# Kernel optimization log

Measured on AMD Instinct MI355X. Metric: run time of the kernel, lower is better.

Reference implementation:

```python
import jax, jax.numpy as jnp
import numpy as np

B, S, H = 8, 1024, 1024
NH, HD = 16, 64
MBANK, TOPK = 128, 16
NLAYERS, FF = 12, 4096
EPS = 1e-5


def _ln(x, w, b):
    m = x.mean(-1, keepdims=True)
    v = ((x - m) ** 2).mean(-1, keepdims=True)
    return (x - m) / jnp.sqrt(v + EPS) * w + b


def _split_heads(x):  # [B,S,H] -> [B,NH,S,HD]
    return x.reshape(B, S, NH, HD).transpose(0, 2, 1, 3)


def _sdpa(q, k, v):  # inputs [B,NH,S,HD]
    scores = jnp.einsum('bhqd,bhkd->bhqk', q, k) / jnp.sqrt(jnp.float32(HD))
    attn = jax.nn.softmax(scores, axis=-1)
    o = jnp.einsum('bhqk,bhkd->bhqd', attn, v)
    return o.transpose(0, 2, 1, 3).reshape(B, S, H)


def setup_inputs() -> dict:
    key = jax.random.key(0)
    ks = jax.random.split(key, 24)
    n = lambda k, shp, s=0.02: jax.random.normal(k, shp, jnp.float32) * s
    return {
        'hidden_states': jax.random.normal(ks[0], (B, S, H), jnp.float32),
        'ln1_w': jnp.ones((H,), jnp.float32), 'ln1_b': jnp.zeros((H,), jnp.float32),
        'ln2_w': jnp.ones((H,), jnp.float32), 'ln2_b': jnp.zeros((H,), jnp.float32),
        'rec_wq': n(ks[1], (H, H)), 'rec_wk': n(ks[2], (H, H)),
        'rec_wv': n(ks[3], (H, H)), 'rec_wo': n(ks[4], (H, H)),
        'rec_ad_w1': n(ks[5], (H // 4, H)), 'rec_ad_w2': n(ks[6], (H, H // 4)),
        'mem_bank': n(ks[7], (MBANK, H)),
        'alloc_w': n(ks[8], (MBANK, H)), 'alloc_b': jnp.zeros((MBANK,), jnp.float32),
        'retr_w': n(ks[9], (MBANK, H)), 'retr_b': jnp.zeros((MBANK,), jnp.float32),
        'upd_w': n(ks[10], (H, H)), 'upd_b': jnp.zeros((H,), jnp.float32),
        'mem_scales': jnp.full((NLAYERS,), 0.1, jnp.float32),
        'attn_in_w': n(ks[11], (3 * H, H)), 'attn_in_b': jnp.zeros((3 * H,), jnp.float32),
        'attn_out_w': n(ks[12], (H, H)), 'attn_out_b': jnp.zeros((H,), jnp.float32),
        'mlp_w1': n(ks[13], (FF, H)), 'mlp_b1': jnp.zeros((FF,), jnp.float32),
        'mlp_w2': n(ks[14], (H, FF)), 'mlp_b2': jnp.zeros((H,), jnp.float32),
        'layer_idx': 4,
    }


def reference(hidden_states, ln1_w, ln1_b, ln2_w, ln2_b,
              rec_wq, rec_wk, rec_wv, rec_wo, rec_ad_w1, rec_ad_w2,
              mem_bank, alloc_w, alloc_b, retr_w, retr_b, upd_w, upd_b, mem_scales,
              attn_in_w, attn_in_b, attn_out_w, attn_out_b,
              mlp_w1, mlp_b1, mlp_w2, mlp_b2, layer_idx):
    residual = hidden_states
    h = _ln(hidden_states, ln1_w, ln1_b)

    # --- CrossLayerParameterRecycler (layer_idx % 4 == 0 and > 0 -> recycle) ---
    if layer_idx % 4 == 0 and layer_idx > 0:
        q = _split_heads(h @ rec_wq.T)
        k = _split_heads(h @ rec_wk.T)
        v = _split_heads(h @ rec_wv.T)
        base_out = _sdpa(q, k, v) @ rec_wo.T
        h = jax.nn.relu(base_out @ rec_ad_w1.T) @ rec_ad_w2.T

    # --- CrossLayerMemoryManager ---
    pooled = h.mean(axis=1)                                  # [B,H]
    alloc_weights = jax.nn.softmax(pooled @ alloc_w.T + alloc_b, axis=-1)   # [B,MBANK]
    retr_weights = jax.nn.softmax(pooled @ retr_w.T + retr_b, axis=-1)
    retrieved = retr_weights @ mem_bank                      # [B,H]
    h = h + retrieved[:, None, :] * mem_scales[layer_idx]
    update_signals = jax.nn.sigmoid(h.mean(axis=1) @ upd_w.T + upd_b)       # [B,H]
    _, top_idx = jax.lax.top_k(alloc_weights, TOPK)          # [B,TOPK]

    # sequential per-batch scatter (later batches overwrite earlier, as in torch loop)
    def _write(mb, be):
        idx, sig = be
        return mb.at[idx].set(jnp.broadcast_to(sig, (TOPK, H))), None
    new_mem_bank, _ = jax.lax.scan(_write, mem_bank, (top_idx, update_signals))

    # --- self attention (nn.MultiheadAttention, batch_first) ---
    qkv = h @ attn_in_w.T + attn_in_b                        # [B,S,3H]
    q, k, v = jnp.split(qkv, 3, axis=-1)
    attn_out = _sdpa(_split_heads(q), _split_heads(k), _split_heads(v))
    attn_out = attn_out @ attn_out_w.T + attn_out_b
    h = residual + attn_out

    # --- MLP block ---
    residual2 = h
    h = _ln(h, ln2_w, ln2_b)
    h = jax.nn.gelu(h @ mlp_w1.T + mlp_b1, approximate=False) @ mlp_w2.T + mlp_b2
    out = residual2 + h
    return out, new_mem_bank
```

## Files before the change

### kernel.cpp

```cpp
#include <hip/hip_runtime.h>
#include <hip/hip_bf16.h>
#include <math.h>
#include <stdint.h>


#define BB 8
#define SS 1024
#define HH 1024
#define NHEAD 16
#define HD 64
#define MBANK 128
#define TOPK_N 16
#define FF_DIM 4096
#define MROWS (BB * SS)
#define NB_ELEM (8ull*1024*1024)

typedef __bf16 bf16x8 __attribute__((ext_vector_type(8)));
typedef __bf16 bf16x4 __attribute__((ext_vector_type(4)));
typedef float f32x4 __attribute__((ext_vector_type(4)));

#define SCALE_LOG2E 0.18033688011112042f

__device__ __forceinline__ unsigned short f2b(float x) {
  unsigned u = __float_as_uint(x);
  unsigned r = (u + 0x7FFFu + ((u >> 16) & 1u)) >> 16;
  return (unsigned short)r;
}
__device__ __forceinline__ float b2f(unsigned short u) {
  return __uint_as_float((unsigned)u << 16);
}

__device__ __forceinline__ float hmax4(f32x4 v) {
  return fmaxf(fmaxf(v[0], v[1]), fmaxf(v[2], v[3]));
}

__device__ __forceinline__ void load16_lds(const void* g, void* lds_base, int lane) {
#if __has_builtin(__builtin_amdgcn_global_load_lds)
  typedef const __attribute__((address_space(1))) unsigned int guint;
  typedef __attribute__((address_space(3))) unsigned int luint;
  __builtin_amdgcn_global_load_lds((guint*)(uintptr_t)g,
                                   (luint*)(unsigned long long)(unsigned int)(uintptr_t)lds_base,
                                   16, 0, 0);
#else
  *(uint4*)((char*)lds_base + lane * 16) = *(const uint4*)g;
#endif
}

__device__ __forceinline__ float gelu_exact(float x) {
  return 0.5f * x * (1.f + erff(x * 0.70710678118654752440f));
}


__global__ __launch_bounds__(256) void cast_split(const float* __restrict__ s,
                                                  unsigned short* __restrict__ hi,
                                                  unsigned short* __restrict__ lo, int n4) {
  int i = blockIdx.x * 256 + threadIdx.x;
  if (i < n4) {
    float4 v = ((const float4*)s)[i];
    ushort4 h, l;
    h.x = f2b(v.x); l.x = f2b(v.x - b2f(h.x));
    h.y = f2b(v.y); l.y = f2b(v.y - b2f(h.y));
    h.z = f2b(v.z); l.z = f2b(v.z - b2f(h.z));
    h.w = f2b(v.w); l.w = f2b(v.w - b2f(h.w));
    ((ushort4*)hi)[i] = h;
    ((ushort4*)lo)[i] = l;
  }
}

__global__ __launch_bounds__(256) void ln3(const float* __restrict__ x,
                                           const float* __restrict__ w,
                                           const float* __restrict__ b,
                                           unsigned short* __restrict__ yh,
                                           unsigned short* __restrict__ yl) {
  int row = blockIdx.x;
  const float* xr = x + (size_t)row * HH;
  int t = threadIdx.x;
  float v[4];
  float s = 0.f, ss = 0.f;
#pragma unroll
  for (int i = 0; i < 4; i++) {
    v[i] = xr[t + i * 256];
    s += v[i];
    ss += v[i] * v[i];
  }
  __shared__ float rs[8], rss[8];
  for (int o = 32; o > 0; o >>= 1) {
    s += __shfl_down(s, o, 64);
    ss += __shfl_down(ss, o, 64);
  }
  int wid = t >> 6, lane = t & 63;
  if (lane == 0) { rs[wid] = s; rss[wid] = ss; }
  __syncthreads();
  if (t == 0) {
    float S = rs[0] + rs[1] + rs[2] + rs[3];
    float SSum = rss[0] + rss[1] + rss[2] + rss[3];
    float m = S * (1.f / HH);
    float var = SSum * (1.f / HH) - m * m;
    rs[4] = m;
    rs[5] = rsqrtf(var + 1e-5f);
  }
  __syncthreads();
  float m = rs[4], inv = rs[5];
#pragma unroll
  for (int i = 0; i < 4; i++) {
    int c = t + i * 256;
    float y = (v[i] - m) * inv * w[c] + b[c];
    unsigned short h = f2b(y);
    yh[(size_t)row * HH + c] = h;
    yl[(size_t)row * HH + c] = f2b(y - b2f(h));
  }
}

template <int ACT, int MODE>
__global__ __launch_bounds__(256) void gemm3(const unsigned short* __restrict__ Ah,
                                             const unsigned short* __restrict__ Al, int lda,
                                             const unsigned short* __restrict__ Wh,
                                             const unsigned short* __restrict__ Wl, int ldw,
                                             unsigned short* __restrict__ Oh,
                                             unsigned short* __restrict__ Ol,
                                             float* __restrict__ outF,
                                             int ldo, int K) {
  __shared__ unsigned short Ash[2][128 * 32];
  __shared__ unsigned short Asl[2][128 * 32];
  __shared__ unsigned short Bsh[2][128 * 32];
  __shared__ unsigned short Bsl[2][128 * 32];
  int n0 = blockIdx.x * 128, m0 = blockIdx.y * 128;
  int t = threadIdx.x, w = t >> 6, L = t & 63, quad = L >> 4, l16 = L & 15;
  int wm = w & 1, wn = w >> 1;
  const f32x4 vzero = {0.f, 0.f, 0.f, 0.f};
  f32x4 acc[4][4];
#pragma unroll
  for (int i = 0; i < 4; i++)
#pragma unroll
    for (int j = 0; j < 4; j++) acc[i][j] = vzero;
  int srow = L >> 2;
  int scol = ((L & 3) ^ ((L >> 3) & 3)) * 8;
  int rsw = (l16 >> 1) & 3;

  auto stage = [&](int buf, int k0) {
#pragma unroll
    for (int c = 0; c < 2; c++) {
      int r = (c * 4 + w) * 16 + srow;
      size_t aoff = (size_t)(m0 + r) * lda + k0 + scol;
      size_t boff = (size_t)(n0 + r) * ldw + k0 + scol;
      load16_lds(Ah + aoff, &Ash[buf][(c * 4 + w) * 512], L);
      load16_lds(Al + aoff, &Asl[buf][(c * 4 + w) * 512], L);
      load16_lds(Wh + boff, &Bsh[buf][(c * 4 + w) * 512], L);
      load16_lds(Wl + boff, &Bsl[buf][(c * 4 + w) * 512], L);
    }
  };
  auto compute = [&](int buf) {
    bf16x8 afh[4], afl[4], bfh[4], bfl[4];
#pragma unroll
    for (int i = 0; i < 4; i++) {
      int off = (wm * 64 + i * 16 + l16) * 32 + (quad ^ rsw) * 8;
      afh[i] = *(const bf16x8*)&Ash[buf][off];
      afl[i] = *(const bf16x8*)&Asl[buf][off];
    }
#pragma unroll
    for (int j = 0; j < 4; j++) {
      int off = (wn * 64 + j * 16 + l16) * 32 + (quad ^ rsw) * 8;
      bfh[j] = *(const bf16x8*)&Bsh[buf][off];
      bfl[j] = *(const bf16x8*)&Bsl[buf][off];
    }
#pragma unroll
    for (int i = 0; i < 4; i++)
#pragma unroll
      for (int j = 0; j < 4; j++) {
        acc[i][j] = __builtin_amdgcn_mfma_f32_16x16x32_bf16(afh[i], bfh[j], acc[i][j], 0, 0, 0);
        acc[i][j] = __builtin_amdgcn_mfma_f32_16x16x32_bf16(afh[i], bfl[j], acc[i][j], 0, 0, 0);
        acc[i][j] = __builtin_amdgcn_mfma_f32_16x16x32_bf16(afl[i], bfh[j], acc[i][j], 0, 0, 0);
      }
  };

  stage(0, 0);
  __syncthreads();
  for (int k0 = 0; k0 < K; k0 += 64) {
    stage(1, k0 + 32);
    compute(0);
    __syncthreads();
    if (k0 + 64 < K) stage(0, k0 + 64);
    compute(1);
    __syncthreads();
  }
#pragma unroll
  for (int i = 0; i < 4; i++) {
    int mb = m0 + wm * 64 + i * 16 + quad * 4;
#pragma unroll
    for (int j = 0; j < 4; j++) {
      int n = n0 + wn * 64 + j * 16 + l16;
      if (MODE == 1) {
        ushort4 sh, sl;
        float vv[4];
#pragma unroll
        for (int r = 0; r < 4; r++) {
          float v = acc[i][j][r];
          if (ACT == 1) v = fmaxf(v, 0.f);
          vv[r] = v;
        }
        sh.x = f2b(vv[0]); sl.x = f2b(vv[0] - b2f(sh.x));
        sh.y = f2b(vv[1]); sl.y = f2b(vv[1] - b2f(sh.y));
        sh.z = f2b(vv[2]); sl.z = f2b(vv[2] - b2f(sh.z));
        sh.w = f2b(vv[3]); sl.w = f2b(vv[3] - b2f(sh.w));
        *(ushort4*)&Oh[(size_t)n * ldo + mb] = sh;
        *(ushort4*)&Ol[(size_t)n * ldo + mb] = sl;
      } else {
#pragma unroll
        for (int r = 0; r < 4; r++) {
          float v = acc[i][j][r];
          if (ACT == 1) v = fmaxf(v, 0.f);
          size_t off = (size_t)(mb + r) * ldo + n;
          if (MODE == 0) {
            unsigned short h = f2b(v);
            Oh[off] = h;
            Ol[off] = f2b(v - b2f(h));
          } else {
            outF[off] = v;
          }
        }
      }
    }
  }
}

__global__ __launch_bounds__(256) void sdpa3(const unsigned short* __restrict__ Qh,
                                             const unsigned short* __restrict__ Ql,
                                             const unsigned short* __restrict__ Kh,
                                             const unsigned short* __restrict__ Kl,
                                             const unsigned short* __restrict__ Vth,
                                             const unsigned short* __restrict__ Vtl,
                                             unsigned short* __restrict__ Oh,
                                             unsigned short* __restrict__ Ol) {
  __shared__ unsigned short Ksh[64 * 64];
  __shared__ unsigned short Ksl[64 * 64];
  __shared__ unsigned short Vsh[64 * 64];
  __shared__ unsigned short Vsl[64 * 64];
  int wg = (int)blockIdx.x;
  int swz = (wg & 7) * 256 + (wg >> 3);
  int qt = swz & 15, h = (swz >> 4) & 15, b = swz >> 8;
  int t = threadIdx.x, w = t >> 6, L = t & 63, quad = L >> 4, l16 = L & 15;
  int q0 = qt * 64;
  const f32x4 vzero = {0.f, 0.f, 0.f, 0.f};
  bf16x8 qfh[2], qfl[2];
  {
    size_t qrow = (size_t)(b * SS + q0 + w * 16 + l16);
#pragma unroll
    for (int kh = 0; kh < 2; kh++) {
      size_t off = qrow * HH + h * 64 + kh * 32 + quad * 8;
      qfh[kh] = *(const bf16x8*)&Qh[off];
      qfl[kh] = *(const bf16x8*)&Ql[off];
    }
  }
  float mprev = -1e30f, lsum = 0.f;
  f32x4 oacc[4];
#pragma unroll
  for (int jd = 0; jd < 4; jd++) oacc[jd] = vzero;
  int srow = L >> 3;
  int scolV = ((L & 7) ^ srow) * 8;
  int rbase = ((l16 & 12) << 1) | (l16 & 3);
  int keyK = (l16 & 3) | (((l16 >> 2) & 1) << 2);
  int k7 = l16 & 7;
  for (int k0 = 0; k0 < SS; k0 += 64) {
    __syncthreads();
#pragma unroll
    for (int c = 0; c < 2; c++) {
      int rr = (c * 4 + w) * 8 + srow;
      int scolK = ((L & 7) ^ ((srow & 3) | (((c * 4 + w) & 1) << 2))) * 8;
      size_t koff = (size_t)(b * SS + k0 + rr) * HH + h * 64 + scolK;
      size_t voff = (size_t)(h * 64 + rr) * MROWS + b * SS + k0 + scolV;
      load16_lds(Kh + koff, &Ksh[(c * 4 + w) * 512], L);
      load16_lds(Kl + koff, &Ksl[(c * 4 + w) * 512], L);
      load16_lds(Vth + voff, &Vsh[(c * 4 + w) * 512], L);
      load16_lds(Vtl + voff, &Vsl[(c * 4 + w) * 512], L);
    }
    __syncthreads();
    f32x4 sacc[4];
#pragma unroll
    for (int jn = 0; jn < 4; jn++) sacc[jn] = vzero;
#pragma unroll
    for (int jn = 0; jn < 4; jn++) {
      int rowp = rbase + (jn & 1) * 4 + (jn >> 1) * 32;
#pragma unroll
      for (int kh = 0; kh < 2; kh++) {
        int off = rowp * 64 + (((kh * 4 + quad) ^ keyK) << 3);
        bf16x8 kfh = *(const bf16x8*)&Ksh[off];
        bf16x8 kfl = *(const bf16x8*)&Ksl[off];
        sacc[jn] = __builtin_amdgcn_mfma_f32_16x16x32_bf16(kfh, qfh[kh], sacc[jn], 0, 0, 0);
        sacc[jn] = __builtin_amdgcn_mfma_f32_16x16x32_bf16(kfl, qfh[kh], sacc[jn], 0, 0, 0);
        sacc[jn] = __builtin_amdgcn_mfma_f32_16x16x32_bf16(kfh, qfl[kh], sacc[jn], 0, 0, 0);
      }
    }
    float mt = fmaxf(fmaxf(hmax4(sacc[0]), hmax4(sacc[1])),
                     fmaxf(hmax4(sacc[2]), hmax4(sacc[3])));
    mt = fmaxf(mt, __shfl_xor(mt, 16, 64));
    mt = fmaxf(mt, __shfl_xor(mt, 32, 64));
    float m2 = fmaxf(mprev, mt * SCALE_LOG2E);
    float rs = 0.f;
    bf16x8 pah[2], pal[2];
#pragma unroll
    for (int jn = 0; jn < 4; jn++) {
      int kh = jn >> 1, half = (jn & 1) * 4;
#pragma unroll
      for (int r = 0; r < 4; r++) {
        float p = exp2f(fmaf(sacc[jn][r], SCALE_LOG2E, -m2));
        rs += p;
        __bf16 ph = (__bf16)p;
        pah[kh][half + r] = ph;
        pal[kh][half + r] = (__bf16)(p - (float)ph);
      }
    }
    rs += __shfl_xor(rs, 16, 64);
    rs += __shfl_xor(rs, 32, 64);
    if (__any(m2 != mprev)) {
      float alpha = exp2f(mprev - m2);
      lsum = lsum * alpha + rs;
      float ar[4];
#pragma unroll
      for (int r = 0; r < 4; r++) ar[r] = __shfl(alpha, quad * 4 + r, 16);
#pragma unroll
      for (int jd = 0; jd < 4; jd++)
#pragma unroll
        for (int r = 0; r < 4; r++) oacc[jd][r] *= ar[r];
    } else {
      lsum += rs;
    }
    mprev = m2;
#pragma unroll
    for (int jd = 0; jd < 4; jd++)
#pragma unroll
      for (int kh = 0; kh < 2; kh++) {
        int off = (jd * 16 + l16) * 64 + ((kh * 4 + quad) ^ k7) * 8;
        bf16x8 vfh = *(const bf16x8*)&Vsh[off];
        bf16x8 vfl = *(const bf16x8*)&Vsl[off];
        oacc[jd] = __builtin_amdgcn_mfma_f32_16x16x32_bf16(pah[kh], vfh, oacc[jd], 0, 0, 0);
        oacc[jd] = __builtin_amdgcn_mfma_f32_16x16x32_bf16(pah[kh], vfl, oacc[jd], 0, 0, 0);
        oacc[jd] = __builtin_amdgcn_mfma_f32_16x16x32_bf16(pal[kh], vfh, oacc[jd], 0, 0, 0);
      }
  }
  float inv = 1.f / lsum;
  float invr[4];
#pragma unroll
  for (int r = 0; r < 4; r++) invr[r] = __shfl(inv, quad * 4 + r, 16);
#pragma unroll
  for (int r = 0; r < 4; r++) {
    size_t row = (size_t)(b * SS + q0 + w * 16 + quad * 4 + r);
#pragma unroll
    for (int jd = 0; jd < 4; jd++) {
      float v = oacc[jd][r] * invr[r];
      unsigned short hh = f2b(v);
      size_t off = row * HH + h * 64 + jd * 16 + l16;
      Oh[off] = hh;
      Ol[off] = f2b(v - b2f(hh));
    }
  }
}


__global__ __launch_bounds__(256) void meanpool_kernel(const float* __restrict__ Hb,
                                                       float* __restrict__ P) {
  int cb = blockIdx.x;
  int b = blockIdx.y;
  int t = threadIdx.x;
  int c = (t & 63) + cb * 64;
  int part = t >> 6;
  float s = 0.f;
  const float* p = Hb + ((size_t)b * SS + part * 256) * HH + c;
  for (int j = 0; j < 256; j++) s += p[(size_t)j * HH];
  __shared__ float red[4][64];
  red[part][t & 63] = s;
  __syncthreads();
  if (t < 64) {
    float tot = red[0][t] + red[1][t] + red[2][t] + red[3][t];
    P[b * HH + cb * 64 + t] = tot * (1.f / SS);
  }
}

__global__ __launch_bounds__(256) void memlogits_kernel(const float* __restrict__ P,
                                                        const float* __restrict__ AW,
                                                        const float* __restrict__ ABias,
                                                        const float* __restrict__ RW,
                                                        const float* __restrict__ RBias,
                                                        float* __restrict__ LA,
                                                        float* __restrict__ LR) {
  int m = blockIdx.x, b = blockIdx.y;
  int t = threadIdx.x;
  const float* pr = P + b * HH;
  const float* aw = AW + (size_t)m * HH;
  const float* rw = RW + (size_t)m * HH;
  float sa = 0.f, sr = 0.f;
  for (int i = t; i < HH; i += 256) {
    float pv = pr[i];
    sa = fmaf(pv, aw[i], sa);
    sr = fmaf(pv, rw[i], sr);
  }
  for (int o = 32; o > 0; o >>= 1) {
    sa += __shfl_down(sa, o, 64);
    sr += __shfl_down(sr, o, 64);
  }
  __shared__ float ra[4], rr[4];
  if ((t & 63) == 0) { ra[t >> 6] = sa; rr[t >> 6] = sr; }
  __syncthreads();
  if (t == 0) {
    LA[b * MBANK + m] = ra[0] + ra[1] + ra[2] + ra[3] + ABias[m];
    LR[b * MBANK + m] = rr[0] + rr[1] + rr[2] + rr[3] + RBias[m];
  }
}

__global__ __launch_bounds__(256) void retrieve_kernel(const float* __restrict__ LA,
                                                       const float* __restrict__ LR,
                                                       const float* __restrict__ MB,
                                                       float* __restrict__ RET,
                                                       int* __restrict__ ISTOP) {
  int b = blockIdx.x;
  int t = threadIdx.x;
  __shared__ float rw[MBANK];
  __shared__ float la[MBANK];
  if (t < MBANK) {
    la[t] = LA[b * MBANK + t];
    rw[t] = LR[b * MBANK + t];
  }
  __syncthreads();
  if (t == 0) {
    float mx = -1e30f;
    for (int i = 0; i < MBANK; i++) mx = fmaxf(mx, rw[i]);
    float s = 0.f;
    for (int i = 0; i < MBANK; i++) {
      float e = __expf(rw[i] - mx);
      rw[i] = e;
      s += e;
    }
    float inv = 1.f / s;
    for (int i = 0; i < MBANK; i++) rw[i] *= inv;
  }
  __syncthreads();
  if (t < MBANK) {
    float mine = la[t];
    int rank = 0;
    for (int i = 0; i < MBANK; i++) {
      float o = la[i];
      if (o > mine || (o == mine && i < t)) rank++;
    }
    ISTOP[b * MBANK + t] = (rank < TOPK_N) ? 1 : 0;
  }
  for (int c = t; c < HH; c += 256) {
    float s = 0.f;
    for (int m = 0; m < MBANK; m++) s = fmaf(rw[m], MB[(size_t)m * HH + c], s);
    RET[b * HH + c] = s;
  }
}

__global__ __launch_bounds__(256) void addmem_kernel(float* __restrict__ Hb,
                                                     const float* __restrict__ RET,
                                                     const float* __restrict__ scales,
                                                     const int* __restrict__ lidx) {
  float sc = scales[lidx[0]];
  size_t i = (size_t)blockIdx.x * 256 + threadIdx.x;
  int c = (int)(i & 1023);
  int b = (int)(i >> 20);
  Hb[i] = fmaf(RET[b * HH + c], sc, Hb[i]);
}

__global__ __launch_bounds__(256) void upd_kernel(const float* __restrict__ P2,
                                                  const float* __restrict__ UW,
                                                  const float* __restrict__ UB,
                                                  float* __restrict__ UPD) {
  int n = blockIdx.x, b = blockIdx.y;
  int t = threadIdx.x;
  const float* pr = P2 + b * HH;
  const float* wr = UW + (size_t)n * HH;
  float s = 0.f;
  for (int i = t; i < HH; i += 256) s = fmaf(pr[i], wr[i], s);
  for (int o = 32; o > 0; o >>= 1) s += __shfl_down(s, o, 64);
  __shared__ float red[4];
  if ((t & 63) == 0) red[t >> 6] = s;
  __syncthreads();
  if (t == 0) {
    float tot = red[0] + red[1] + red[2] + red[3] + UB[n];
    UPD[b * HH + n] = 1.f / (1.f + __expf(-tot));
  }
}

__global__ __launch_bounds__(256) void membank_kernel(const float* __restrict__ MB,
                                                      const int* __restrict__ ISTOP,
                                                      const float* __restrict__ UPD,
                                                      float* __restrict__ OUT) {
  int row = blockIdx.x;
  int col = blockIdx.y * 256 + threadIdx.x;
  int w = -1;
  for (int b = 0; b < BB; b++)
    if (ISTOP[b * MBANK + row]) w = b;
  float v = (w >= 0) ? UPD[w * HH + col] : MB[(size_t)row * HH + col];
  OUT[(size_t)row * HH + col] = v;
}


__global__ __launch_bounds__(256) void ln_bf(const float* __restrict__ x,
                                             const float* __restrict__ w,
                                             const float* __restrict__ b,
                                             unsigned short* __restrict__ y) {
  int row = blockIdx.x;
  const float* xr = x + (size_t)row * HH;
  unsigned short* yr = y + (size_t)row * HH;
  int t = threadIdx.x;
  float v[4];
  float s = 0.f, ss = 0.f;
#pragma unroll
  for (int i = 0; i < 4; i++) {
    v[i] = xr[t + i * 256];
    s += v[i];
    ss += v[i] * v[i];
  }
  __shared__ float rs[8], rss[8];
  for (int o = 32; o > 0; o >>= 1) {
    s += __shfl_down(s, o, 64);
    ss += __shfl_down(ss, o, 64);
  }
  int wid = t >> 6, lane = t & 63;
  if (lane == 0) { rs[wid] = s; rss[wid] = ss; }
  __syncthreads();
  if (t == 0) {
    float S = rs[0] + rs[1] + rs[2] + rs[3];
    float SSum = rss[0] + rss[1] + rss[2] + rss[3];
    float m = S * (1.f / HH);
    float var = SSum * (1.f / HH) - m * m;
    rs[4] = m;
    rs[5] = rsqrtf(var + 1e-5f);
  }
  __syncthreads();
  float m = rs[4], inv = rs[5];
#pragma unroll
  for (int i = 0; i < 4; i++) {
    int c = t + i * 256;
    yr[c] = f2b((v[i] - m) * inv * w[c] + b[c]);
  }
}

__global__ __launch_bounds__(256) void castf2b(const float* __restrict__ s,
                                               unsigned short* __restrict__ d, int n4) {
  int i = blockIdx.x * 256 + threadIdx.x;
  if (i < n4) {
    float4 v = ((const float4*)s)[i];
    ushort4 o;
    o.x = f2b(v.x); o.y = f2b(v.y); o.z = f2b(v.z); o.w = f2b(v.w);
    ((ushort4*)d)[i] = o;
  }
}

template <int ACT, int MODE>
__global__ __launch_bounds__(256) void gemm_bf(const unsigned short* __restrict__ A, int lda,
                                               const unsigned short* __restrict__ W, int ldw,
                                               const float* __restrict__ bias,
                                               const float* __restrict__ resid,
                                               float* __restrict__ outF,
                                               unsigned short* __restrict__ outB,
                                               int ldo, int K) {
  __shared__ unsigned short As[2][128 * 32];
  __shared__ unsigned short Bs[2][128 * 32];
  int n0 = blockIdx.x * 128, m0 = blockIdx.y * 128;
  int t = threadIdx.x, w = t >> 6, L = t & 63, quad = L >> 4, l16 = L & 15;
  int wm = w & 1, wn = w >> 1;
  const f32x4 vzero = {0.f, 0.f, 0.f, 0.f};
  f32x4 acc[4][4];
#pragma unroll
  for (int i = 0; i < 4; i++)
#pragma unroll
    for (int j = 0; j < 4; j++) acc[i][j] = vzero;
  int srow = L >> 2;
  int scol = ((L & 3) ^ ((L >> 3) & 3)) * 8;
  int rsw = (l16 >> 1) & 3;

  auto stage = [&](int buf, int k0) {
#pragma unroll
    for (int c = 0; c < 2; c++) {
      int r = (c * 4 + w) * 16 + srow;
      load16_lds(A + (size_t)(m0 + r) * lda + k0 + scol, &As[buf][(c * 4 + w) * 512], L);
      load16_lds(W + (size_t)(n0 + r) * ldw + k0 + scol, &Bs[buf][(c * 4 + w) * 512], L);
    }
  };
  auto compute = [&](int buf) {
    bf16x8 af[4], bfr[4];
#pragma unroll
    for (int i = 0; i < 4; i++)
      af[i] = *(const bf16x8*)&As[buf][(wm * 64 + i * 16 + l16) * 32 + (quad ^ rsw) * 8];
#pragma unroll
    for (int j = 0; j < 4; j++)
      bfr[j] = *(const bf16x8*)&Bs[buf][(wn * 64 + j * 16 + l16) * 32 + (quad ^ rsw) * 8];
#pragma unroll
    for (int i = 0; i < 4; i++)
#pragma unroll
      for (int j = 0; j < 4; j++)
        acc[i][j] = __builtin_amdgcn_mfma_f32_16x16x32_bf16(af[i], bfr[j], acc[i][j], 0, 0, 0);
  };

  stage(0, 0);
  __syncthreads();
  for (int k0 = 0; k0 < K; k0 += 64) {
    stage(1, k0 + 32);
    compute(0);
    __syncthreads();
    if (k0 + 64 < K) stage(0, k0 + 64);
    compute(1);
    __syncthreads();
  }
#pragma unroll
  for (int i = 0; i < 4; i++) {
    int mb = m0 + wm * 64 + i * 16 + quad * 4;
#pragma unroll
    for (int j = 0; j < 4; j++) {
      int n = n0 + wn * 64 + j * 16 + l16;
      float bv = bias ? bias[n] : 0.f;
      if (MODE == 2) {
        ushort4 st;
        float v0 = acc[i][j][0] + bv, v1 = acc[i][j][1] + bv;
        float v2 = acc[i][j][2] + bv, v3 = acc[i][j][3] + bv;
        if (ACT == 1) { v0 = fmaxf(v0, 0.f); v1 = fmaxf(v1, 0.f); v2 = fmaxf(v2, 0.f); v3 = fmaxf(v3, 0.f); }
        if (ACT == 2) { v0 = gelu_exact(v0); v1 = gelu_exact(v1); v2 = gelu_exact(v2); v3 = gelu_exact(v3); }
        st.x = f2b(v0); st.y = f2b(v1); st.z = f2b(v2); st.w = f2b(v3);
        *(ushort4*)&outB[(size_t)n * ldo + mb] = st;
      } else {
#pragma unroll
        for (int r = 0; r < 4; r++) {
          float v = acc[i][j][r] + bv;
          if (ACT == 1) v = fmaxf(v, 0.f);
          if (ACT == 2) v = gelu_exact(v);
          size_t off = (size_t)(mb + r) * ldo + n;
          if (MODE == 1) outB[off] = f2b(v);
          else if (MODE == 3) outF[off] += v;
          else if (MODE == 4) outF[off] = v + resid[off];
        }
      }
    }
  }
}

__global__ __launch_bounds__(256) void sdpa_bf(const unsigned short* __restrict__ Q,
                                               const unsigned short* __restrict__ Kb,
                                               const unsigned short* __restrict__ Vt,
                                               unsigned short* __restrict__ O) {
  __shared__ unsigned short Ks[64 * 64];
  __shared__ unsigned short Vs[64 * 64];
  int wg = (int)blockIdx.x;
  int swz = (wg & 7) * 256 + (wg >> 3);
  int qt = swz & 15, h = (swz >> 4) & 15, b = swz >> 8;
  int t = threadIdx.x, w = t >> 6, L = t & 63, quad = L >> 4, l16 = L & 15;
  int q0 = qt * 64;
  const f32x4 vzero = {0.f, 0.f, 0.f, 0.f};
  bf16x8 qf[2];
  {
    size_t qrow = (size_t)(b * SS + q0 + w * 16 + l16);
#pragma unroll
    for (int kh = 0; kh < 2; kh++)
      qf[kh] = *(const bf16x8*)&Q[qrow * HH + h * 64 + kh * 32 + quad * 8];
  }
  float mprev = -1e30f, lsum = 0.f;
  f32x4 oacc[4];
#pragma unroll
  for (int jd = 0; jd < 4; jd++) oacc[jd] = vzero;
  int srow = L >> 3;
  int scolV = ((L & 7) ^ srow) * 8;
  int rbase = ((l16 & 12) << 1) | (l16 & 3);
  int keyK = (l16 & 3) | (((l16 >> 2) & 1) << 2);
  int k7 = l16 & 7;
  for (int k0 = 0; k0 < SS; k0 += 64) {
    __syncthreads();
#pragma unroll
    for (int c = 0; c < 2; c++) {
      int rr = (c * 4 + w) * 8 + srow;
      int scolK = ((L & 7) ^ ((srow & 3) | (((c * 4 + w) & 1) << 2))) * 8;
      load16_lds(Kb + (size_t)(b * SS + k0 + rr) * HH + h * 64 + scolK, &Ks[(c * 4 + w) * 512], L);
      load16_lds(Vt + (size_t)(h * 64 + rr) * MROWS + b * SS + k0 + scolV, &Vs[(c * 4 + w) * 512], L);
    }
    __syncthreads();
    f32x4 sacc[4];
#pragma unroll
    for (int jn = 0; jn < 4; jn++) sacc[jn] = vzero;
#pragma unroll
    for (int jn = 0; jn < 4; jn++) {
      int rowp = rbase + (jn & 1) * 4 + (jn >> 1) * 32;
#pragma unroll
      for (int kh = 0; kh < 2; kh++) {
        bf16x8 kf = *(const bf16x8*)&Ks[rowp * 64 + (((kh * 4 + quad) ^ keyK) << 3)];
        sacc[jn] = __builtin_amdgcn_mfma_f32_16x16x32_bf16(kf, qf[kh], sacc[jn], 0, 0, 0);
      }
    }
    float mt = fmaxf(fmaxf(hmax4(sacc[0]), hmax4(sacc[1])),
                     fmaxf(hmax4(sacc[2]), hmax4(sacc[3])));
    mt = fmaxf(mt, __shfl_xor(mt, 16, 64));
    mt = fmaxf(mt, __shfl_xor(mt, 32, 64));
    float m2 = fmaxf(mprev, mt * SCALE_LOG2E);
    float rs = 0.f;
    bf16x8 pa[2];
#pragma unroll
    for (int jn = 0; jn < 4; jn++) {
      int kh = jn >> 1, half = (jn & 1) * 4;
#pragma unroll
      for (int r = 0; r < 4; r++) {
        float p = exp2f(fmaf(sacc[jn][r], SCALE_LOG2E, -m2));
        rs += p;
        pa[kh][half + r] = (__bf16)p;
      }
    }
    rs += __shfl_xor(rs, 16, 64);
    rs += __shfl_xor(rs, 32, 64);
    if (__any(m2 != mprev)) {
      float alpha = exp2f(mprev - m2);
      lsum = lsum * alpha + rs;
      float ar[4];
#pragma unroll
      for (int r = 0; r < 4; r++) ar[r] = __shfl(alpha, quad * 4 + r, 16);
#pragma unroll
      for (int jd = 0; jd < 4; jd++)
#pragma unroll
        for (int r = 0; r < 4; r++) oacc[jd][r] *= ar[r];
    } else {
      lsum += rs;
    }
    mprev = m2;
#pragma unroll
    for (int jd = 0; jd < 4; jd++)
#pragma unroll
      for (int kh = 0; kh < 2; kh++) {
        bf16x8 vf = *(const bf16x8*)&Vs[(jd * 16 + l16) * 64 + ((kh * 4 + quad) ^ k7) * 8];
        oacc[jd] = __builtin_amdgcn_mfma_f32_16x16x32_bf16(pa[kh], vf, oacc[jd], 0, 0, 0);
      }
  }
  float inv = 1.f / lsum;
  float invr[4];
#pragma unroll
  for (int r = 0; r < 4; r++) invr[r] = __shfl(inv, quad * 4 + r, 16);
#pragma unroll
  for (int r = 0; r < 4; r++) {
    size_t row = (size_t)(b * SS + q0 + w * 16 + quad * 4 + r);
#pragma unroll
    for (int jd = 0; jd < 4; jd++)
      O[row * HH + h * 64 + jd * 16 + l16] = f2b(oacc[jd][r] * invr[r]);
  }
}

extern "C" void kernel_launch(void* const* d_in, const int* in_sizes, int n_in,
                              void* d_out, int out_size, void* d_ws, size_t ws_size,
                              hipStream_t stream) {
  const float* x = (const float*)d_in[0];
  const float* ln1_w = (const float*)d_in[1];
  const float* ln1_b = (const float*)d_in[2];
  const float* ln2_w = (const float*)d_in[3];
  const float* ln2_b = (const float*)d_in[4];
  const float* rec_wq = (const float*)d_in[5];
  const float* rec_wk = (const float*)d_in[6];
  const float* rec_wv = (const float*)d_in[7];
  const float* rec_wo = (const float*)d_in[8];
  const float* rec_ad_w1 = (const float*)d_in[9];
  const float* rec_ad_w2 = (const float*)d_in[10];
  const float* mem_bank = (const float*)d_in[11];
  const float* alloc_w = (const float*)d_in[12];
  const float* alloc_b = (const float*)d_in[13];
  const float* retr_w = (const float*)d_in[14];
  const float* retr_b = (const float*)d_in[15];
  const float* upd_w = (const float*)d_in[16];
  const float* upd_b = (const float*)d_in[17];
  const float* mem_scales = (const float*)d_in[18];
  const float* attn_in_w = (const float*)d_in[19];
  const float* attn_in_b = (const float*)d_in[20];
  const float* attn_out_w = (const float*)d_in[21];
  const float* attn_out_b = (const float*)d_in[22];
  const float* mlp_w1 = (const float*)d_in[23];
  const float* mlp_b1 = (const float*)d_in[24];
  const float* mlp_w2 = (const float*)d_in[25];
  const float* mlp_b2 = (const float*)d_in[26];
  const int* layer_idx = (const int*)d_in[27];

  float* out = (float*)d_out;
  float* out_mb = out + NB_ELEM;

  const size_t U = NB_ELEM;
  unsigned short* W16 = (unsigned short*)d_ws;
  unsigned short* U0 = W16;
  unsigned short* U1 = W16 + U;
  unsigned short* U2 = W16 + 2 * U;
  unsigned short* U3 = W16 + 3 * U;
  unsigned short* U4 = W16 + 4 * U;
  unsigned short* U5 = W16 + 5 * U;
  unsigned short* wsh = W16 + 6 * U;
  unsigned short* wsl = wsh + 1048576;
  float* small = (float*)(wsl + 1048576);
  float* pooled = small;
  float* pooled2 = small + 8192;
  float* logitsA = small + 16384;
  float* logitsR = small + 17408;
  float* retrieved = small + 18432;
  float* updsig = small + 26624;
  int* istop = (int*)(small + 34816);
  unsigned short* D0 = (unsigned short*)out;
  unsigned short* D1 = D0 + U;
  unsigned short* ain_bf = U5;
  unsigned short* aout_bf = U5 + 3 * 1048576;

  dim3 blk(256);
  dim3 gG(8, 64);
  dim3 gG256(2, 64);
  dim3 gS1(2048);
  const int EW_GRID = (int)(NB_ELEM / 256);

  ln3<<<MROWS, blk, 0, stream>>>(x, ln1_w, ln1_b, U0, U1);
  cast_split<<<1024, blk, 0, stream>>>(rec_wq, wsh, wsl, 262144);
  gemm3<0, 0><<<gG, blk, 0, stream>>>(U0, U1, HH, wsh, wsl, HH, U2, U3, nullptr, HH, HH);
  cast_split<<<1024, blk, 0, stream>>>(rec_wk, wsh, wsl, 262144);
  gemm3<0, 0><<<gG, blk, 0, stream>>>(U0, U1, HH, wsh, wsl, HH, U4, U5, nullptr, HH, HH);
  cast_split<<<1024, blk, 0, stream>>>(rec_wv, wsh, wsl, 262144);
  gemm3<0, 1><<<gG, blk, 0, stream>>>(U0, U1, HH, wsh, wsl, HH, D0, D1, nullptr, MROWS, HH);
  sdpa3<<<gS1, blk, 0, stream>>>(U2, U3, U4, U5, D0, D1, U0, U1);
  cast_split<<<1024, blk, 0, stream>>>(rec_wo, wsh, wsl, 262144);
  gemm3<0, 0><<<gG, blk, 0, stream>>>(U0, U1, HH, wsh, wsl, HH, U2, U3, nullptr, HH, HH);
  cast_split<<<256, blk, 0, stream>>>(rec_ad_w1, wsh, wsl, 65536);
  gemm3<1, 0><<<gG256, blk, 0, stream>>>(U2, U3, HH, wsh, wsl, HH, U4, U4 + 2097152, nullptr, 256, HH);
  cast_split<<<256, blk, 0, stream>>>(rec_ad_w2, wsh, wsl, 65536);
  gemm3<0, 2><<<gG, blk, 0, stream>>>(U4, U4 + 2097152, 256, wsh, wsl, 256, nullptr, nullptr, out, HH, 256);
  meanpool_kernel<<<dim3(HH / 64, BB), blk, 0, stream>>>(out, pooled);
  memlogits_kernel<<<dim3(MBANK, BB), blk, 0, stream>>>(pooled, alloc_w, alloc_b, retr_w, retr_b, logitsA, logitsR);
  retrieve_kernel<<<BB, blk, 0, stream>>>(logitsA, logitsR, mem_bank, retrieved, istop);
  addmem_kernel<<<EW_GRID, blk, 0, stream>>>(out, retrieved, mem_scales, layer_idx);
  meanpool_kernel<<<dim3(HH / 64, BB), blk, 0, stream>>>(out, pooled2);
  upd_kernel<<<dim3(HH, BB), blk, 0, stream>>>(pooled2, upd_w, upd_b, updsig);
  membank_kernel<<<dim3(MBANK, HH / 256), blk, 0, stream>>>(mem_bank, istop, updsig, out_mb);
  castf2b<<<8192, blk, 0, stream>>>(out, U0, 2097152);
  castf2b<<<3072, blk, 0, stream>>>(attn_in_w, ain_bf, 786432);
  castf2b<<<1024, blk, 0, stream>>>(attn_out_w, aout_bf, 262144);
  gemm_bf<0, 1><<<gG, blk, 0, stream>>>(U0, HH, ain_bf, HH, attn_in_b, nullptr, nullptr, U1, HH, HH);
  gemm_bf<0, 1><<<gG, blk, 0, stream>>>(U0, HH, ain_bf + (size_t)HH * HH, HH, attn_in_b + HH, nullptr, nullptr, U2, HH, HH);
  gemm_bf<0, 2><<<gG, blk, 0, stream>>>(U0, HH, ain_bf + 2ull * HH * HH, HH, attn_in_b + 2 * HH, nullptr, nullptr, U3, MROWS, HH);
  sdpa_bf<<<gS1, blk, 0, stream>>>(U1, U2, U3, U4);
  gemm_bf<0, 4><<<gG, blk, 0, stream>>>(U4, HH, aout_bf, HH, attn_out_b, x, out, nullptr, HH, HH);
  ln_bf<<<MROWS, blk, 0, stream>>>(out, ln2_w, ln2_b, U1);
  {
    unsigned short* w1b = U0;
    unsigned short* w2b = U0 + 4 * 1048576;
    unsigned short* h2 = U2;
    castf2b<<<4096, blk, 0, stream>>>(mlp_w1, w1b, 1048576);
    castf2b<<<4096, blk, 0, stream>>>(mlp_w2, w2b, 1048576);
    gemm_bf<2, 1><<<dim3(32, 64), blk, 0, stream>>>(U1, HH, w1b, HH, mlp_b1, nullptr, nullptr, h2, FF_DIM, HH);
    gemm_bf<0, 3><<<gG, blk, 0, stream>>>(h2, FF_DIM, w2b, FF_DIM, mlp_b2, nullptr, out, nullptr, HH, FF_DIM);
  }
}
```

Baseline: 1.126 ms.

## Process two 64-row query tiles per attention block to reuse K/V tiles

Both flash-attention kernels (the split-precision sdpa3 and the bf16 sdpa_bf) now give each workgroup 128 query rows, as two 64-row sub-tiles with separate online-softmax state. Each K/V tile loaded into shared memory is therefore used twice, which halves global K/V traffic and the number of barriers per query row. The grid shrinks from 2048 to 1024 blocks and register use per thread roughly doubles for Q fragments and accumulators, which may lower occupancy.

```diff
diff --git a/kernel.cpp b/kernel.cpp
--- a/kernel.cpp
+++ b/kernel.cpp
@@ -236,25 +236,28 @@
   __shared__ unsigned short Vsh[64 * 64];
   __shared__ unsigned short Vsl[64 * 64];
   int wg = (int)blockIdx.x;
-  int swz = (wg & 7) * 256 + (wg >> 3);
-  int qt = swz & 15, h = (swz >> 4) & 15, b = swz >> 8;
+  int swz = (wg & 7) * 128 + (wg >> 3);
+  int qt = swz & 7, h = (swz >> 3) & 15, b = swz >> 7;
   int t = threadIdx.x, w = t >> 6, L = t & 63, quad = L >> 4, l16 = L & 15;
-  int q0 = qt * 64;
+  int q0 = qt * 128;
   const f32x4 vzero = {0.f, 0.f, 0.f, 0.f};
-  bf16x8 qfh[2], qfl[2];
-  {
-    size_t qrow = (size_t)(b * SS + q0 + w * 16 + l16);
+  bf16x8 qfh[2][2], qfl[2][2];
+#pragma unroll
+  for (int qs = 0; qs < 2; qs++) {
+    size_t qrow = (size_t)(b * SS + q0 + qs * 64 + w * 16 + l16);
 #pragma unroll
     for (int kh = 0; kh < 2; kh++) {
       size_t off = qrow * HH + h * 64 + kh * 32 + quad * 8;
-      qfh[kh] = *(const bf16x8*)&Qh[off];
-      qfl[kh] = *(const bf16x8*)&Ql[off];
-    }
-  }
-  float mprev = -1e30f, lsum = 0.f;
-  f32x4 oacc[4];
-#pragma unroll
-  for (int jd = 0; jd < 4; jd++) oacc[jd] = vzero;
+      qfh[qs][kh] = *(const bf16x8*)&Qh[off];
+      qfl[qs][kh] = *(const bf16x8*)&Ql[off];
+    }
+  }
+  float mprev[2] = {-1e30f, -1e30f}, lsum[2] = {0.f, 0.f};
+  f32x4 oacc[2][4];
+#pragma unroll
+  for (int qs = 0; qs < 2; qs++)
+#pragma unroll
+    for (int jd = 0; jd < 4; jd++) oacc[qs][jd] = vzero;
   int srow = L >> 3;
   int scolV = ((L & 7) ^ srow) * 8;
   int rbase = ((l16 & 12) << 1) | (l16 & 3);
@@ -274,83 +277,89 @@
       load16_lds(Vtl + voff, &Vsl[(c * 4 + w) * 512], L);
     }
     __syncthreads();
-    f32x4 sacc[4];
-#pragma unroll
-    for (int jn = 0; jn < 4; jn++) sacc[jn] = vzero;
-#pragma unroll
-    for (int jn = 0; jn < 4; jn++) {
-      int rowp = rbase + (jn & 1) * 4 + (jn >> 1) * 32;
-#pragma unroll
-      for (int kh = 0; kh < 2; kh++) {
-        int off = rowp * 64 + (((kh * 4 + quad) ^ keyK) << 3);
-        bf16x8 kfh = *(const bf16x8*)&Ksh[off];
-        bf16x8 kfl = *(const bf16x8*)&Ksl[off];
-        sacc[jn] = __builtin_amdgcn_mfma_f32_16x16x32_bf16(kfh, qfh[kh], sacc[jn], 0, 0, 0);
-        sacc[jn] = __builtin_amdgcn_mfma_f32_16x16x32_bf16(kfl, qfh[kh], sacc[jn], 0, 0, 0);
-        sacc[jn] = __builtin_amdgcn_mfma_f32_16x16x32_bf16(kfh, qfl[kh], sacc[jn], 0, 0, 0);
-      }
-    }
-    float mt = fmaxf(fmaxf(hmax4(sacc[0]), hmax4(sacc[1])),
-                     fmaxf(hmax4(sacc[2]), hmax4(sacc[3])));
-    mt = fmaxf(mt, __shfl_xor(mt, 16, 64));
-    mt = fmaxf(mt, __shfl_xor(mt, 32, 64));
-    float m2 = fmaxf(mprev, mt * SCALE_LOG2E);
-    float rs = 0.f;
-    bf16x8 pah[2], pal[2];
-#pragma unroll
-    for (int jn = 0; jn < 4; jn++) {
-      int kh = jn >> 1, half = (jn & 1) * 4;
-#pragma unroll
-      for (int r = 0; r < 4; r++) {
-        float p = exp2f(fmaf(sacc[jn][r], SCALE_LOG2E, -m2));
-        rs += p;
-        __bf16 ph = (__bf16)p;
-        pah[kh][half + r] = ph;
-        pal[kh][half + r] = (__bf16)(p - (float)ph);
-      }
-    }
-    rs += __shfl_xor(rs, 16, 64);
-    rs += __shfl_xor(rs, 32, 64);
-    if (__any(m2 != mprev)) {
-      float alpha = exp2f(mprev - m2);
-      lsum = lsum * alpha + rs;
-      float ar[4];
-#pragma unroll
-      for (int r = 0; r < 4; r++) ar[r] = __shfl(alpha, quad * 4 + r, 16);
+#pragma unroll
+    for (int qs = 0; qs < 2; qs++) {
+      f32x4 sacc[4];
+#pragma unroll
+      for (int jn = 0; jn < 4; jn++) sacc[jn] = vzero;
+#pragma unroll
+      for (int jn = 0; jn < 4; jn++) {
+        int rowp = rbase + (jn & 1) * 4 + (jn >> 1) * 32;
+#pragma unroll
+        for (int kh = 0; kh < 2; kh++) {
+          int off = rowp * 64 + (((kh * 4 + quad) ^ keyK) << 3);
+          bf16x8 kfh = *(const bf16x8*)&Ksh[off];
+          bf16x8 kfl = *(const bf16x8*)&Ksl[off];
+          sacc[jn] = __builtin_amdgcn_mfma_f32_16x16x32_bf16(kfh, qfh[qs][kh], sacc[jn], 0, 0, 0);
+          sacc[jn] = __builtin_amdgcn_mfma_f32_16x16x32_bf16(kfl, qfh[qs][kh], sacc[jn], 0, 0, 0);
+          sacc[jn] = __builtin_amdgcn_mfma_f32_16x16x32_bf16(kfh, qfl[qs][kh], sacc[jn], 0, 0, 0);
+        }
+      }
+      float mt = fmaxf(fmaxf(hmax4(sacc[0]), hmax4(sacc[1])),
+                       fmaxf(hmax4(sacc[2]), hmax4(sacc[3])));
+      mt = fmaxf(mt, __shfl_xor(mt, 16, 64));
+      mt = fmaxf(mt, __shfl_xor(mt, 32, 64));
+      float m2 = fmaxf(mprev[qs], mt * SCALE_LOG2E);
+      float rs = 0.f;
+      bf16x8 pah[2], pal[2];
+#pragma unroll
+      for (int jn = 0; jn < 4; jn++) {
+        int kh = jn >> 1, half = (jn & 1) * 4;
+#pragma unroll
+        for (int r = 0; r < 4; r++) {
+          float p = exp2f(fmaf(sacc[jn][r], SCALE_LOG2E, -m2));
+          rs += p;
+          __bf16 ph = (__bf16)p;
+          pah[kh][half + r] = ph;
+          pal[kh][half + r] = (__bf16)(p - (float)ph);
+        }
+      }
+      rs += __shfl_xor(rs, 16, 64);
+      rs += __shfl_xor(rs, 32, 64);
+      if (__any(m2 != mprev[qs])) {
+        float alpha = exp2f(mprev[qs] - m2);
+        lsum[qs] = lsum[qs] * alpha + rs;
+        float ar[4];
+#pragma unroll
+        for (int r = 0; r < 4; r++) ar[r] = __shfl(alpha, quad * 4 + r, 16);
+#pragma unroll
+        for (int jd = 0; jd < 4; jd++)
+#pragma unroll
+          for (int r = 0; r < 4; r++) oacc[qs][jd][r] *= ar[r];
+      } else {
+        lsum[qs] += rs;
+      }
+      mprev[qs] = m2;
 #pragma unroll
       for (int jd = 0; jd < 4; jd++)
 #pragma unroll
-        for (int r = 0; r < 4; r++) oacc[jd][r] *= ar[r];
-    } else {
-      lsum += rs;
-    }
-    mprev = m2;
-#pragma unroll
-    for (int jd = 0; jd < 4; jd++)
-#pragma unroll
-      for (int kh = 0; kh < 2; kh++) {
-        int off = (jd * 16 + l16) * 64 + ((kh * 4 + quad) ^ k7) * 8;
-        bf16x8 vfh = *(const bf16x8*)&Vsh[off];
-        bf16x8 vfl = *(const bf16x8*)&Vsl[off];
-        oacc[jd] = __builtin_amdgcn_mfma_f32_16x16x32_bf16(pah[kh], vfh, oacc[jd], 0, 0, 0);
-        oacc[jd] = __builtin_amdgcn_mfma_f32_16x16x32_bf16(pah[kh], vfl, oacc[jd], 0, 0, 0);
-        oacc[jd] = __builtin_amdgcn_mfma_f32_16x16x32_bf16(pal[kh], vfh, oacc[jd], 0, 0, 0);
-      }
-  }
-  float inv = 1.f / lsum;
-  float invr[4];
-#pragma unroll
-  for (int r = 0; r < 4; r++) invr[r] = __shfl(inv, quad * 4 + r, 16);
-#pragma unroll
-  for (int r = 0; r < 4; r++) {
-    size_t row = (size_t)(b * SS + q0 + w * 16 + quad * 4 + r);
-#pragma unroll
-    for (int jd = 0; jd < 4; jd++) {
-      float v = oacc[jd][r] * invr[r];
-      unsigned short hh = f2b(v);
-      size_t off = row * HH + h * 64 + jd * 16 + l16;
-      Oh[off] = hh;
-      Ol[off] = f2b(v - b2f(hh));
+        for (int kh = 0; kh < 2; kh++) {
+          int off = (jd * 16 + l16) * 64 + ((kh * 4 + quad) ^ k7) * 8;
+          bf16x8 vfh = *(const bf16x8*)&Vsh[off];
+          bf16x8 vfl = *(const bf16x8*)&Vsl[off];
+          oacc[qs][jd] = __builtin_amdgcn_mfma_f32_16x16x32_bf16(pah[kh], vfh, oacc[qs][jd], 0, 0, 0);
+          oacc[qs][jd] = __builtin_amdgcn_mfma_f32_16x16x32_bf16(pah[kh], vfl, oacc[qs][jd], 0, 0, 0);
+          oacc[qs][jd] = __builtin_amdgcn_mfma_f32_16x16x32_bf16(pal[kh], vfh, oacc[qs][jd], 0, 0, 0);
+        }
+    }
+  }
+#pragma unroll
+  for (int qs = 0; qs < 2; qs++) {
+    float inv = 1.f / lsum[qs];
+    float invr[4];
+#pragma unroll
+    for (int r = 0; r < 4; r++) invr[r] = __shfl(inv, quad * 4 + r, 16);
+#pragma unroll
+    for (int r = 0; r < 4; r++) {
+      size_t row = (size_t)(b * SS + q0 + qs * 64 + w * 16 + quad * 4 + r);
+#pragma unroll
+      for (int jd = 0; jd < 4; jd++) {
+        float v = oacc[qs][jd][r] * invr[r];
+        unsigned short hh = f2b(v);
+        size_t off = row * HH + h * 64 + jd * 16 + l16;
+        Oh[off] = hh;
+        Ol[off] = f2b(v - b2f(hh));
+      }
     }
   }
 }
@@ -640,22 +649,25 @@
   __shared__ unsigned short Ks[64 * 64];
   __shared__ unsigned short Vs[64 * 64];
   int wg = (int)blockIdx.x;
-  int swz = (wg & 7) * 256 + (wg >> 3);
-  int qt = swz & 15, h = (swz >> 4) & 15, b = swz >> 8;
+  int swz = (wg & 7) * 128 + (wg >> 3);
+  int qt = swz & 7, h = (swz >> 3) & 15, b = swz >> 7;
   int t = threadIdx.x, w = t >> 6, L = t & 63, quad = L >> 4, l16 = L & 15;
-  int q0 = qt * 64;
+  int q0 = qt * 128;
   const f32x4 vzero = {0.f, 0.f, 0.f, 0.f};
-  bf16x8 qf[2];
-  {
-    size_t qrow = (size_t)(b * SS + q0 + w * 16 + l16);
+  bf16x8 qf[2][2];
+#pragma unroll
+  for (int qs = 0; qs < 2; qs++) {
+    size_t qrow = (size_t)(b * SS + q0 + qs * 64 + w * 16 + l16);
 #pragma unroll
     for (int kh = 0; kh < 2; kh++)
-      qf[kh] = *(const bf16x8*)&Q[qrow * HH + h * 64 + kh * 32 + quad * 8];
-  }
-  float mprev = -1e30f, lsum = 0.f;
-  f32x4 oacc[4];
-#pragma unroll
-  for (int jd = 0; jd < 4; jd++) oacc[jd] = vzero;
+      qf[qs][kh] = *(const bf16x8*)&Q[qrow * HH + h * 64 + kh * 32 + quad * 8];
+  }
+  float mprev[2] = {-1e30f, -1e30f}, lsum[2] = {0.f, 0.f};
+  f32x4 oacc[2][4];
+#pragma unroll
+  for (int qs = 0; qs < 2; qs++)
+#pragma unroll
+    for (int jd = 0; jd < 4; jd++) oacc[qs][jd] = vzero;
   int srow = L >> 3;
   int scolV = ((L & 7) ^ srow) * 8;
   int rbase = ((l16 & 12) << 1) | (l16 & 3);
@@ -671,69 +683,75 @@
       load16_lds(Vt + (size_t)(h * 64 + rr) * MROWS + b * SS + k0 + scolV, &Vs[(c * 4 + w) * 512], L);
     }
     __syncthreads();
-    f32x4 sacc[4];
-#pragma unroll
-    for (int jn = 0; jn < 4; jn++) sacc[jn] = vzero;
-#pragma unroll
-    for (int jn = 0; jn < 4; jn++) {
-      int rowp = rbase + (jn & 1) * 4 + (jn >> 1) * 32;
-#pragma unroll
-      for (int kh = 0; kh < 2; kh++) {
-        bf16x8 kf = *(const bf16x8*)&Ks[rowp * 64 + (((kh * 4 + quad) ^ keyK) << 3)];
-        sacc[jn] = __builtin_amdgcn_mfma_f32_16x16x32_bf16(kf, qf[kh], sacc[jn], 0, 0, 0);
-      }
-    }
-    float mt = fmaxf(fmaxf(hmax4(sacc[0]), hmax4(sacc[1])),
-                     fmaxf(hmax4(sacc[2]), hmax4(sacc[3])));
-    mt = fmaxf(mt, __shfl_xor(mt, 16, 64));
-    mt = fmaxf(mt, __shfl_xor(mt, 32, 64));
-    float m2 = fmaxf(mprev, mt * SCALE_LOG2E);
-    float rs = 0.f;
-    bf16x8 pa[2];
-#pragma unroll
-    for (int jn = 0; jn < 4; jn++) {
-      int kh = jn >> 1, half = (jn & 1) * 4;
-#pragma unroll
-      for (int r = 0; r < 4; r++) {
-        float p = exp2f(fmaf(sacc[jn][r], SCALE_LOG2E, -m2));
-        rs += p;
-        pa[kh][half + r] = (__bf16)p;
-      }
-    }
-    rs += __shfl_xor(rs, 16, 64);
-    rs += __shfl_xor(rs, 32, 64);
-    if (__any(m2 != mprev)) {
-      float alpha = exp2f(mprev - m2);
-      lsum = lsum * alpha + rs;
-      float ar[4];
-#pragma unroll
-      for (int r = 0; r < 4; r++) ar[r] = __shfl(alpha, quad * 4 + r, 16);
+#pragma unroll
+    for (int qs = 0; qs < 2; qs++) {
+      f32x4 sacc[4];
+#pragma unroll
+      for (int jn = 0; jn < 4; jn++) sacc[jn] = vzero;
+#pragma unroll
+      for (int jn = 0; jn < 4; jn++) {
+        int rowp = rbase + (jn & 1) * 4 + (jn >> 1) * 32;
+#pragma unroll
+        for (int kh = 0; kh < 2; kh++) {
+          bf16x8 kf = *(const bf16x8*)&Ks[rowp * 64 + (((kh * 4 + quad) ^ keyK) << 3)];
+          sacc[jn] = __builtin_amdgcn_mfma_f32_16x16x32_bf16(kf, qf[qs][kh], sacc[jn], 0, 0, 0);
+        }
+      }
+      float mt = fmaxf(fmaxf(hmax4(sacc[0]), hmax4(sacc[1])),
+                       fmaxf(hmax4(sacc[2]), hmax4(sacc[3])));
+      mt = fmaxf(mt, __shfl_xor(mt, 16, 64));
+      mt = fmaxf(mt, __shfl_xor(mt, 32, 64));
+      float m2 = fmaxf(mprev[qs], mt * SCALE_LOG2E);
+      float rs = 0.f;
+      bf16x8 pa[2];
+#pragma unroll
+      for (int jn = 0; jn < 4; jn++) {
+        int kh = jn >> 1, half = (jn & 1) * 4;
+#pragma unroll
+        for (int r = 0; r < 4; r++) {
+          float p = exp2f(fmaf(sacc[jn][r], SCALE_LOG2E, -m2));
+          rs += p;
+          pa[kh][half + r] = (__bf16)p;
+        }
+      }
+      rs += __shfl_xor(rs, 16, 64);
+      rs += __shfl_xor(rs, 32, 64);
+      if (__any(m2 != mprev[qs])) {
+        float alpha = exp2f(mprev[qs] - m2);
+        lsum[qs] = lsum[qs] * alpha + rs;
+        float ar[4];
+#pragma unroll
+        for (int r = 0; r < 4; r++) ar[r] = __shfl(alpha, quad * 4 + r, 16);
+#pragma unroll
+        for (int jd = 0; jd < 4; jd++)
+#pragma unroll
+          for (int r = 0; r < 4; r++) oacc[qs][jd][r] *= ar[r];
+      } else {
+        lsum[qs] += rs;
+      }
+      mprev[qs] = m2;
 #pragma unroll
       for (int jd = 0; jd < 4; jd++)
 #pragma unroll
-        for (int r = 0; r < 4; r++) oacc[jd][r] *= ar[r];
-    } else {
-      lsum += rs;
-    }
-    mprev = m2;
-#pragma unroll
-    for (int jd = 0; jd < 4; jd++)
-#pragma unroll
-      for (int kh = 0; kh < 2; kh++) {
-        bf16x8 vf = *(const bf16x8*)&Vs[(jd * 16 + l16) * 64 + ((kh * 4 + quad) ^ k7) * 8];
-        oacc[jd] = __builtin_amdgcn_mfma_f32_16x16x32_bf16(pa[kh], vf, oacc[jd], 0, 0, 0);
-      }
-  }
-  float inv = 1.f / lsum;
-  float invr[4];
-#pragma unroll
-  for (int r = 0; r < 4; r++) invr[r] = __shfl(inv, quad * 4 + r, 16);
-#pragma unroll
-  for (int r = 0; r < 4; r++) {
-    size_t row = (size_t)(b * SS + q0 + w * 16 + quad * 4 + r);
-#pragma unroll
-    for (int jd = 0; jd < 4; jd++)
-      O[row * HH + h * 64 + jd * 16 + l16] = f2b(oacc[jd][r] * invr[r]);
+        for (int kh = 0; kh < 2; kh++) {
+          bf16x8 vf = *(const bf16x8*)&Vs[(jd * 16 + l16) * 64 + ((kh * 4 + quad) ^ k7) * 8];
+          oacc[qs][jd] = __builtin_amdgcn_mfma_f32_16x16x32_bf16(pa[kh], vf, oacc[qs][jd], 0, 0, 0);
+        }
+    }
+  }
+#pragma unroll
+  for (int qs = 0; qs < 2; qs++) {
+    float inv = 1.f / lsum[qs];
+    float invr[4];
+#pragma unroll
+    for (int r = 0; r < 4; r++) invr[r] = __shfl(inv, quad * 4 + r, 16);
+#pragma unroll
+    for (int r = 0; r < 4; r++) {
+      size_t row = (size_t)(b * SS + q0 + qs * 64 + w * 16 + quad * 4 + r);
+#pragma unroll
+      for (int jd = 0; jd < 4; jd++)
+        O[row * HH + h * 64 + jd * 16 + l16] = f2b(oacc[qs][jd][r] * invr[r]);
+    }
   }
 }
 
@@ -798,7 +816,7 @@
   dim3 blk(256);
   dim3 gG(8, 64);
   dim3 gG256(2, 64);
-  dim3 gS1(2048);
+  dim3 gS2(1024);
   const int EW_GRID = (int)(NB_ELEM / 256);
 
   ln3<<<MROWS, blk, 0, stream>>>(x, ln1_w, ln1_b, U0, U1);
@@ -808,7 +826,7 @@
   gemm3<0, 0><<<gG, blk, 0, stream>>>(U0, U1, HH, wsh, wsl, HH, U4, U5, nullptr, HH, HH);
   cast_split<<<1024, blk, 0, stream>>>(rec_wv, wsh, wsl, 262144);
   gemm3<0, 1><<<gG, blk, 0, stream>>>(U0, U1, HH, wsh, wsl, HH, D0, D1, nullptr, MROWS, HH);
-  sdpa3<<<gS1, blk, 0, stream>>>(U2, U3, U4, U5, D0, D1, U0, U1);
+  sdpa3<<<gS2, blk, 0, stream>>>(U2, U3, U4, U5, D0, D1, U0, U1);
   cast_split<<<1024, blk, 0, stream>>>(rec_wo, wsh, wsl, 262144);
   gemm3<0, 0><<<gG, blk, 0, stream>>>(U0, U1, HH, wsh, wsl, HH, U2, U3, nullptr, HH, HH);
   cast_split<<<256, blk, 0, stream>>>(rec_ad_w1, wsh, wsl, 65536);
@@ -828,7 +846,7 @@
   gemm_bf<0, 1><<<gG, blk, 0, stream>>>(U0, HH, ain_bf, HH, attn_in_b, nullptr, nullptr, U1, HH, HH);
   gemm_bf<0, 1><<<gG, blk, 0, stream>>>(U0, HH, ain_bf + (size_t)HH * HH, HH, attn_in_b + HH, nullptr, nullptr, U2, HH, HH);
   gemm_bf<0, 2><<<gG, blk, 0, stream>>>(U0, HH, ain_bf + 2ull * HH * HH, HH, attn_in_b + 2 * HH, nullptr, nullptr, U3, MROWS, HH);
-  sdpa_bf<<<gS1, blk, 0, stream>>>(U1, U2, U3, U4);
+  sdpa_bf<<<gS2, blk, 0, stream>>>(U1, U2, U3, U4);
   gemm_bf<0, 4><<<gG, blk, 0, stream>>>(U4, HH, aout_bf, HH, attn_out_b, x, out, nullptr, HH, HH);
   ln_bf<<<MROWS, blk, 0, stream>>>(out, ln2_w, ln2_b, U1);
   {
```

Measured after the change: 1.149 ms. 2.0% more time.
